# Performance work log

Measured on AMD Instinct MI355X. Metric: run time of the kernel, lower is better.

The kernel has to match this reference:

```python
import jax, jax.numpy as jnp
import numpy as np

B, L, D = 4, 8192, 1024
EPS = 1e-4


def setup_inputs() -> dict:
    key = jax.random.key(0)
    k1, k2, k3 = jax.random.split(key, 3)
    hidden_states = jax.random.normal(k1, (B, L, D), dtype=jnp.float32)  # (B, M=L, D)
    boundary_mask = jax.random.randint(k2, (B, L), 0, 2).astype(bool)
    boundary_mask = boundary_mask.at[:, 0].set(True)  # first token is always a boundary
    boundary_prob = jax.random.uniform(k3, (B, L, 2), dtype=jnp.float32)
    return {
        "hidden_states": hidden_states,
        "boundary_mask": boundary_mask,
        "boundary_prob": boundary_prob,
    }


def reference(hidden_states, boundary_mask, boundary_prob):
    # plug_back_idx: index of the chunk each position belongs to
    idx = jnp.cumsum(boundary_mask.astype(jnp.int32), axis=1) - 1  # (B, L)
    # expand chunk representations back to full sequence length
    expanded = jnp.take_along_axis(hidden_states, idx[:, :, None], axis=1).astype(jnp.float32)  # (B, L, D)
    p = jnp.clip(boundary_prob[..., -1].astype(jnp.float32), EPS, 1.0 - EPS)  # (B, L)
    # torch code: out_0 = x_0 exactly (p[:,0] unused); encode as p_0 = 1 with zero init state
    p = p.at[:, 0].set(1.0)
    # EMA recurrence out_t = p_t * x_t + (1 - p_t) * out_{t-1} as a log-depth
    # associative scan over affine maps y -> a*y + b.
    a = (1.0 - p)[:, :, None]            # (B, L, 1)
    b = p[:, :, None] * expanded          # (B, L, D)

    def combine(e1, e2):
        a1, b1 = e1
        a2, b2 = e2
        return a1 * a2, a2 * b1 + b2

    _, out = jax.lax.associative_scan(combine, (a, b), axis=1)
    return out  # (B, L, D) float32, matching out.to(original_dtype)
```

## Files before the change

### kernel.cpp

```cpp
#include <hip/hip_runtime.h>

#define NB 4
#define LL 8192
#define DD 1024
#define CHUNK 64
#define NT (LL / CHUNK)
#define NF (NB * NT)
#define EPSV 1e-4f
#define WCUT 1e-7f

__global__ __launch_bounds__(1024) void k_one(const float* __restrict__ hid,
                                              const void* __restrict__ mask_raw,
                                              const float* __restrict__ bprob,
                                              float* __restrict__ out) {
    const int blk0 = blockIdx.x;
    const int f = (blk0 & 7) * (NF / 8) + (blk0 >> 3);
    const int b = f >> 7;
    const int T = f & (NT - 1);
    const int l0 = T * CHUNK;
    const int tid = threadIdx.x;
    const int lane = tid & 63, wv = tid >> 6;

    __shared__ int   s_viol;
    __shared__ int   s_wsum[16];
    __shared__ int   s_excl[1024];
    __shared__ int   s_i[2][CHUNK];
    __shared__ float s_pv[2][CHUNK];
    __shared__ int   s_ls;

    if (tid == 0) s_viol = 0;
    __syncthreads();
    {
        unsigned int w = ((const unsigned int*)mask_raw)[tid];
        if ((w & 0xFFFFFF00u) != 0u || (w & 0xFFu) > 1u) atomicOr(&s_viol, 1);
    }
    __syncthreads();
    const bool is_int = (s_viol == 0);

    const int e0 = b * LL + tid * 8;
    int s = 0;
    if (is_int) {
        const int4* mi = (const int4*)((const int*)mask_raw + e0);
        #pragma unroll
        for (int k = 0; k < 2; ++k) { int4 q = mi[k]; s += q.x + q.y + q.z + q.w; }
    } else {
        const unsigned int* mb = (const unsigned int*)((const unsigned char*)mask_raw + e0);
        #pragma unroll
        for (int k = 0; k < 2; ++k) s += (int)((mb[k] * 0x01010101u) >> 24);
    }
    int v = s;
    #pragma unroll
    for (int off = 1; off < 64; off <<= 1) {
        int u = __shfl_up(v, off, 64);
        if (lane >= off) v += u;
    }
    if (lane == 63) s_wsum[wv] = v;
    __syncthreads();
    int wexcl = 0;
    #pragma unroll
    for (int i = 0; i < 16; ++i) if (i < wv) wexcl += s_wsum[i];
    s_excl[tid] = wexcl + (v - s);

    if (wv == 0) {
        int ls = T;
        float cum = 1.f;
        while (ls > 0 && cum > WCUT) {
            --ls;
            const int l = ls * CHUNK + lane;
            float pv = bprob[((size_t)(b * LL + l)) * 2 + 1];
            pv = fminf(fmaxf(pv, EPSV), 1.0f - EPSV);
            if (l == 0) pv = 1.0f;
            float P = 1.f - pv;
            #pragma unroll
            for (int off = 1; off < 64; off <<= 1)
                P *= __shfl_xor(P, off, 64);
            cum *= P;
        }
        if (lane == 0) s_ls = ls;
    }
    __syncthreads();
    const int ls = s_ls;

    const float* hb = hid + (size_t)b * LL * DD + tid;
    float* ob = out + ((size_t)b * LL + l0) * DD + tid;
    float y = 0.f;
    for (int c = ls; c <= T; ++c) {
        const int slot = c & 1;
        if (wv == 0) {
            const int cs = c * CHUNK;
            int mval;
            if (is_int) mval = ((const int*)mask_raw)[b * LL + cs + lane];
            else        mval = (int)((const unsigned char*)mask_raw)[b * LL + cs + lane];
            int cc = mval;
            #pragma unroll
            for (int off = 1; off < 64; off <<= 1) {
                int u = __shfl_up(cc, off, 64);
                if (lane >= off) cc += u;
            }
            s_i[slot][lane] = s_excl[c * 8] + cc - 1;
            const int l = cs + lane;
            float pv = bprob[((size_t)(b * LL + l)) * 2 + 1];
            pv = fminf(fmaxf(pv, EPSV), 1.0f - EPSV);
            if (l == 0) pv = 1.0f;
            s_pv[slot][lane] = pv;
        }
        __syncthreads();
        if (c < T) {
            #pragma unroll 8
            for (int t = 0; t < CHUNK; ++t) {
                const float p = s_pv[slot][t];
                const float x = hb[(size_t)s_i[slot][t] * DD];
                y = fmaf(p, x, (1.f - p) * y);
            }
        } else {
            #pragma unroll 8
            for (int t = 0; t < CHUNK; ++t) {
                const float p = s_pv[slot][t];
                const float x = hb[(size_t)s_i[slot][t] * DD];
                y = fmaf(p, x, (1.f - p) * y);
                __builtin_nontemporal_store(y, &ob[(size_t)t * DD]);
            }
        }
    }
}

extern "C" void kernel_launch(void* const* d_in, const int* in_sizes, int n_in,
                              void* d_out, int out_size, void* d_ws, size_t ws_size,
                              hipStream_t stream) {
    const float* hid   = (const float*)d_in[0];
    const void*  mask  = d_in[1];
    const float* bprob = (const float*)d_in[2];
    float* out = (float*)d_out;

    k_one<<<NF, 1024, 0, stream>>>(hid, mask, bprob, out);
}
```

Before: 46.61 us.

## Collapse warm-up recurrence into weighted sum over distinct prior chunk rows

Each block's warm-up used to replay the EMA recurrence over whole previous chunks until the decay product fell below a cutoff, reading a full hidden row for every position. Now a second wave computes suffix products of (1-p) over the preceding chunk and finds where decay passes the cutoff. It accumulates per-row weights in shared memory, keyed by gathered row index, so the initial state is a short dot product over only the distinct rows referenced. This removes redundant gathers for repeated rows and drops the serial dependency chain. If the cutoff is not reached within one chunk, it falls back to the old multi-chunk loop.

```diff
diff --git a/kernel.cpp b/kernel.cpp
--- a/kernel.cpp
+++ b/kernel.cpp
@@ -26,9 +26,11 @@
     __shared__ int   s_excl[1024];
     __shared__ int   s_i[2][CHUNK];
     __shared__ float s_pv[2][CHUNK];
-    __shared__ int   s_ls;
-
-    if (tid == 0) s_viol = 0;
+    __shared__ float s_w[CHUNK];
+    __shared__ int   s_r0w, s_nrw, s_fb, s_ls;
+
+    if (tid == 0) { s_viol = 0; s_fb = 0; s_nrw = 0; }
+    if (tid < CHUNK) s_w[tid] = 0.f;
     __syncthreads();
     {
         unsigned int w = ((const unsigned int*)mask_raw)[tid];
@@ -60,65 +62,136 @@
     #pragma unroll
     for (int i = 0; i < 16; ++i) if (i < wv) wexcl += s_wsum[i];
     s_excl[tid] = wexcl + (v - s);
+    __syncthreads();
 
     if (wv == 0) {
-        int ls = T;
-        float cum = 1.f;
-        while (ls > 0 && cum > WCUT) {
-            --ls;
-            const int l = ls * CHUNK + lane;
-            float pv = bprob[((size_t)(b * LL + l)) * 2 + 1];
-            pv = fminf(fmaxf(pv, EPSV), 1.0f - EPSV);
-            if (l == 0) pv = 1.0f;
-            float P = 1.f - pv;
-            #pragma unroll
-            for (int off = 1; off < 64; off <<= 1)
-                P *= __shfl_xor(P, off, 64);
-            cum *= P;
-        }
-        if (lane == 0) s_ls = ls;
-    }
-    __syncthreads();
-    const int ls = s_ls;
+        int mval;
+        if (is_int) mval = ((const int*)mask_raw)[b * LL + l0 + lane];
+        else        mval = (int)((const unsigned char*)mask_raw)[b * LL + l0 + lane];
+        int cc = mval;
+        #pragma unroll
+        for (int off = 1; off < 64; off <<= 1) {
+            int u = __shfl_up(cc, off, 64);
+            if (lane >= off) cc += u;
+        }
+        s_i[0][lane] = s_excl[T * 8] + cc - 1;
+        const int l = l0 + lane;
+        float pv = bprob[((size_t)(b * LL + l)) * 2 + 1];
+        pv = fminf(fmaxf(pv, EPSV), 1.0f - EPSV);
+        if (l == 0) pv = 1.0f;
+        s_pv[0][lane] = pv;
+    }
+    if (wv == 1 && T > 0) {
+        const int lw = l0 - CHUNK + lane;
+        int mval;
+        if (is_int) mval = ((const int*)mask_raw)[b * LL + lw];
+        else        mval = (int)((const unsigned char*)mask_raw)[b * LL + lw];
+        int cc = mval;
+        #pragma unroll
+        for (int off = 1; off < 64; off <<= 1) {
+            int u = __shfl_up(cc, off, 64);
+            if (lane >= off) cc += u;
+        }
+        const int my_idx = s_excl[(T - 1) * 8] + cc - 1;
+
+        float pv = bprob[((size_t)(b * LL + lw)) * 2 + 1];
+        pv = fminf(fmaxf(pv, EPSV), 1.0f - EPSV);
+        if (lw == 0) pv = 1.0f;
+        const float a = 1.f - pv;
+        float P = a;
+        #pragma unroll
+        for (int off = 1; off < 64; off <<= 1) {
+            float u = __shfl_down(P, off, 64);
+            if (lane < 64 - off) P *= u;
+        }
+        float S = __shfl_down(P, 1, 64);
+        if (lane == 63) S = 1.f;
+
+        const unsigned long long cut = __ballot(P <= WCUT);
+        if (cut != 0ull) {
+            const int lstar = 63 - __clzll(cut);
+            const int r0w   = __shfl(my_idx, lstar, 64);
+            const int rlast = __shfl(my_idx, 63, 64);
+            if (lane >= lstar) atomicAdd(&s_w[my_idx - r0w], pv * S);
+            if (lane == 0) { s_r0w = r0w; s_nrw = rlast - r0w + 1; }
+        } else {
+            float cum = __shfl(P, 0, 64);
+            int ls = T - 1;
+            while (ls > 0 && cum > WCUT) {
+                --ls;
+                const int l2 = ls * CHUNK + lane;
+                float pv2 = bprob[((size_t)(b * LL + l2)) * 2 + 1];
+                pv2 = fminf(fmaxf(pv2, EPSV), 1.0f - EPSV);
+                if (l2 == 0) pv2 = 1.0f;
+                float P2 = 1.f - pv2;
+                #pragma unroll
+                for (int off = 1; off < 64; off <<= 1)
+                    P2 *= __shfl_xor(P2, off, 64);
+                cum *= P2;
+            }
+            if (lane == 0) { s_fb = 1; s_ls = ls; }
+        }
+    }
+    __syncthreads();
 
     const float* hb = hid + (size_t)b * LL * DD + tid;
     float* ob = out + ((size_t)b * LL + l0) * DD + tid;
-    float y = 0.f;
-    for (int c = ls; c <= T; ++c) {
-        const int slot = c & 1;
-        if (wv == 0) {
-            const int cs = c * CHUNK;
-            int mval;
-            if (is_int) mval = ((const int*)mask_raw)[b * LL + cs + lane];
-            else        mval = (int)((const unsigned char*)mask_raw)[b * LL + cs + lane];
-            int cc = mval;
-            #pragma unroll
-            for (int off = 1; off < 64; off <<= 1) {
-                int u = __shfl_up(cc, off, 64);
-                if (lane >= off) cc += u;
+
+    if (!s_fb) {
+        float y = 0.f;
+        const int nrw = s_nrw;
+        if (nrw > 0) {
+            const float* hw = hb + (size_t)s_r0w * DD;
+            #pragma unroll 4
+            for (int r = 0; r < nrw; ++r)
+                y = fmaf(s_w[r], hw[(size_t)r * DD], y);
+        }
+        #pragma unroll 8
+        for (int t = 0; t < CHUNK; ++t) {
+            const float p = s_pv[0][t];
+            const float x = hb[(size_t)s_i[0][t] * DD];
+            y = fmaf(p, x, (1.f - p) * y);
+            __builtin_nontemporal_store(y, &ob[(size_t)t * DD]);
+        }
+    } else {
+        const int ls = s_ls;
+        float y = 0.f;
+        for (int c = ls; c <= T; ++c) {
+            const int slot = c & 1;
+            if (wv == 0) {
+                const int cs = c * CHUNK;
+                int mval;
+                if (is_int) mval = ((const int*)mask_raw)[b * LL + cs + lane];
+                else        mval = (int)((const unsigned char*)mask_raw)[b * LL + cs + lane];
+                int cc = mval;
+                #pragma unroll
+                for (int off = 1; off < 64; off <<= 1) {
+                    int u = __shfl_up(cc, off, 64);
+                    if (lane >= off) cc += u;
+                }
+                s_i[slot][lane] = s_excl[c * 8] + cc - 1;
+                const int l = cs + lane;
+                float pv = bprob[((size_t)(b * LL + l)) * 2 + 1];
+                pv = fminf(fmaxf(pv, EPSV), 1.0f - EPSV);
+                if (l == 0) pv = 1.0f;
+                s_pv[slot][lane] = pv;
             }
-            s_i[slot][lane] = s_excl[c * 8] + cc - 1;
-            const int l = cs + lane;
-            float pv = bprob[((size_t)(b * LL + l)) * 2 + 1];
-            pv = fminf(fmaxf(pv, EPSV), 1.0f - EPSV);
-            if (l == 0) pv = 1.0f;
-            s_pv[slot][lane] = pv;
-        }
-        __syncthreads();
-        if (c < T) {
-            #pragma unroll 8
-            for (int t = 0; t < CHUNK; ++t) {
-                const float p = s_pv[slot][t];
-                const float x = hb[(size_t)s_i[slot][t] * DD];
-                y = fmaf(p, x, (1.f - p) * y);
-            }
-        } else {
-            #pragma unroll 8
-            for (int t = 0; t < CHUNK; ++t) {
-                const float p = s_pv[slot][t];
-                const float x = hb[(size_t)s_i[slot][t] * DD];
-                y = fmaf(p, x, (1.f - p) * y);
-                __builtin_nontemporal_store(y, &ob[(size_t)t * DD]);
+            __syncthreads();
+            if (c < T) {
+                #pragma unroll 8
+                for (int t = 0; t < CHUNK; ++t) {
+                    const float p = s_pv[slot][t];
+                    const float x = hb[(size_t)s_i[slot][t] * DD];
+                    y = fmaf(p, x, (1.f - p) * y);
+                }
+            } else {
+                #pragma unroll 8
+                for (int t = 0; t < CHUNK; ++t) {
+                    const float p = s_pv[slot][t];
+                    const float x = hb[(size_t)s_i[slot][t] * DD];
+                    y = fmaf(p, x, (1.f - p) * y);
+                    __builtin_nontemporal_store(y, &ob[(size_t)t * DD]);
+                }
             }
         }
     }
```

Result: faster. 39.14 us (-16.0%).
